# Kernel tuning notes

Hardware: AMD Instinct MI355X
Metric: run time of the kernel (lower is better)

The kernel has to match this reference:

```python
import jax, jax.numpy as jnp
import numpy as np
from jax import lax

V, B, T, H = 8000, 64, 128, 512
EMB_INIT = 0.5 / 128.0  # init_width = 0.5 / embedding_size


def setup_inputs() -> dict:
    key = jax.random.key(0)
    ks = jax.random.split(key, 9)
    return {
        "input_data": jax.random.randint(ks[0], (B, T), 0, V, dtype=jnp.int64),
        "targets": jax.random.randint(ks[1], (B, T), 0, V, dtype=jnp.int64),
        "embedding": jax.random.uniform(ks[2], (V, H), minval=-EMB_INIT, maxval=EMB_INIT, dtype=jnp.float32),
        "W1": jax.random.normal(ks[3], (2 * H, 4 * H), dtype=jnp.float32) * 0.02,
        "b1": jnp.zeros((4 * H,), dtype=jnp.float32),
        "W2": jax.random.normal(ks[4], (2 * H, 4 * H), dtype=jnp.float32) * 0.02,
        "b2": jnp.zeros((4 * H,), dtype=jnp.float32),
        "softmax_w": jax.random.normal(ks[5], (H, V), dtype=jnp.float32) * 0.02,
        "softmax_b": jnp.zeros((V,), dtype=jnp.float32),
    }


def _lstm_step(c, h, x, W, b):
    # BasicLSTMCell with forget_bias=0.0, gate order i, j, f, o
    gates = jnp.concatenate([x, h], axis=-1) @ W + b  # [B, 4H]
    i, j, f, o = jnp.split(gates, 4, axis=-1)
    c_new = c * jax.nn.sigmoid(f) + jax.nn.sigmoid(i) * jnp.tanh(j)
    h_new = jnp.tanh(c_new) * jax.nn.sigmoid(o)
    return c_new, h_new


def reference(input_data, targets, embedding, W1, b1, W2, b2, softmax_w, softmax_b):
    x = embedding[input_data]            # [B, T, H] embedding lookup
    xt = jnp.transpose(x, (1, 0, 2))     # [T, B, H] time-major for scan

    def step(carry, x_t):
        c1, h1, c2, h2 = carry
        c1, h1 = _lstm_step(c1, h1, x_t, W1, b1)
        c2, h2 = _lstm_step(c2, h2, h1, W2, b2)
        return (c1, h1, c2, h2), h2

    init = tuple(jnp.zeros((B, H), dtype=x.dtype) for _ in range(4))
    _, hs = lax.scan(step, init, xt)     # [T, B, H]

    outputs = jnp.transpose(hs, (1, 0, 2)).reshape(-1, H)  # [B*T, H]
    logits = outputs @ softmax_w + softmax_b               # [B*T, V]
    labels = targets.reshape(-1)                            # [B*T]

    logp = jax.nn.log_softmax(logits, axis=-1)
    loss = -jnp.take_along_axis(logp, labels[:, None], axis=1)[:, 0]  # per-token CE
    cost = jnp.sum(loss) / (B * T)
    return cost
```

## Files before the change

### kernel.cpp

```cpp
#include <hip/hip_runtime.h>
#include <hip/hip_bf16.h>


#define V_SIZE 8000
#define B_SIZE 64
#define T_SIZE 128
#define H_SIZE 512
#define NG     (4 * H_SIZE)
#define HB     (H_SIZE * B_SIZE)
#define RBLK   64
#define RTH    256
#define SENT   0x7FFF7FFFu

typedef __attribute__((ext_vector_type(8))) short bf16x8;
typedef __attribute__((ext_vector_type(8))) unsigned short u16x8;
typedef __attribute__((ext_vector_type(4))) float f32x4;

__device__ __forceinline__ float bf2f(unsigned short u) {
  union { unsigned int i; float f; } x; x.i = ((unsigned int)u) << 16; return x.f;
}
__device__ __forceinline__ unsigned short f2bf(float f) {
  union { float f; unsigned int i; } x; x.f = f;
  unsigned int r = x.i + 0x7fffu + ((x.i >> 16) & 1u);
  return (unsigned short)(r >> 16);
}
__device__ __forceinline__ float sigf(float v) { return 1.f / (1.f + __expf(-v)); }
__device__ __forceinline__ float tanhf_fast(float v) {
  return 1.f - 2.f / (__expf(2.f * v) + 1.f);
}

__device__ __forceinline__ bf16x8 aload16(const unsigned short* p) {
  unsigned long long lo = __hip_atomic_load((const unsigned long long*)p,
                                            __ATOMIC_RELAXED, __HIP_MEMORY_SCOPE_AGENT);
  unsigned long long hi = __hip_atomic_load((const unsigned long long*)(p + 4),
                                            __ATOMIC_RELAXED, __HIP_MEMORY_SCOPE_AGENT);
  union { unsigned long long v[2]; bf16x8 b; } u;
  u.v[0] = lo; u.v[1] = hi;
  return u.b;
}
__device__ __forceinline__ unsigned has_sent(bf16x8 v) {
  union { bf16x8 b; unsigned u[4]; } x; x.b = v;
  return (unsigned)((x.u[0] == SENT) | (x.u[1] == SENT) |
                    (x.u[2] == SENT) | (x.u[3] == SENT));
}

__device__ __forceinline__ void load8_mall(bf16x8* d, const unsigned short* base) {
  asm volatile(
      "global_load_dwordx4 %0, %8, off sc0 sc1\n\t"
      "global_load_dwordx4 %1, %8, off offset:64 sc0 sc1\n\t"
      "global_load_dwordx4 %2, %8, off offset:128 sc0 sc1\n\t"
      "global_load_dwordx4 %3, %8, off offset:192 sc0 sc1\n\t"
      "global_load_dwordx4 %4, %8, off offset:256 sc0 sc1\n\t"
      "global_load_dwordx4 %5, %8, off offset:320 sc0 sc1\n\t"
      "global_load_dwordx4 %6, %8, off offset:384 sc0 sc1\n\t"
      "global_load_dwordx4 %7, %8, off offset:448 sc0 sc1\n\t"
      "s_waitcnt vmcnt(0)"
      : "=v"(d[0]), "=v"(d[1]), "=v"(d[2]), "=v"(d[3]),
        "=v"(d[4]), "=v"(d[5]), "=v"(d[6]), "=v"(d[7])
      : "v"(base)
      : "memory");
}

__global__ void fill_k(unsigned* __restrict__ p, unsigned v, int n) {
  int i = blockIdx.x * 256 + threadIdx.x;
  if (i < n) p[i] = v;
}

__global__ __launch_bounds__(256) void xgather_k(const int* __restrict__ ids,
                                                 const float* __restrict__ emb,
                                                 unsigned short* __restrict__ xb) {
  int g = blockIdx.x * 256 + threadIdx.x;
  int r = g >> 6, c = g & 63;
  int t = r >> 6, b = r & 63;
  int id = ids[(size_t)b * T_SIZE + t];
  const float4* s4 = reinterpret_cast<const float4*>(emb + (size_t)id * H_SIZE + c * 8);
  float4 v0 = s4[0], v1 = s4[1];
  u16x8 o;
  o[0] = f2bf(v0.x); o[1] = f2bf(v0.y); o[2] = f2bf(v0.z); o[3] = f2bf(v0.w);
  o[4] = f2bf(v1.x); o[5] = f2bf(v1.y); o[6] = f2bf(v1.z); o[7] = f2bf(v1.w);
  *reinterpret_cast<u16x8*>(xb + (size_t)r * H_SIZE + c * 8) = o;
}

__global__ __launch_bounds__(256) void trans_k(const float* __restrict__ src,
                                               unsigned short* __restrict__ dst,
                                               int src_ld, int n_tiles) {
  __shared__ float tile[64][65];
  const int tid = threadIdx.x;
  const int kt = blockIdx.x / n_tiles, nt = blockIdx.x % n_tiles;
#pragma unroll
  for (int q = 0; q < 16; ++q) {
    int f = tid + 256 * q;
    int r = f >> 6, c = f & 63;
    tile[r][c] = src[(size_t)(kt * 64 + r) * src_ld + nt * 64 + c];
  }
  __syncthreads();
#pragma unroll
  for (int q = 0; q < 2; ++q) {
    int u = tid + 256 * q;
    int n = u >> 3, kg = u & 7;
    u16x8 o;
#pragma unroll
    for (int e = 0; e < 8; ++e) o[e] = f2bf(tile[kg * 8 + e][n]);
    *reinterpret_cast<u16x8*>(dst + (size_t)(nt * 64 + n) * 512 + kt * 64 + kg * 8) = o;
  }
}

__device__ __forceinline__ void loadB8(bf16x8* p, const unsigned short* Wb,
                                       int vc, int kh, int kof) {
#pragma unroll
  for (int ks = 0; ks < 8; ++ks)
    p[ks] = *reinterpret_cast<const bf16x8*>(
        Wb + (size_t)vc * 512 + (kh * 8 + ks) * 32 + kof);
}

__global__ __launch_bounds__(RTH, 1) void recur_k(
    const float* __restrict__ W1, const float* __restrict__ W2,
    const float* __restrict__ b1, const float* __restrict__ b2,
    const unsigned short* __restrict__ xb,
    const unsigned short* __restrict__ hzero,
    unsigned short* __restrict__ h1all, unsigned short* __restrict__ h2all)
{
  __shared__ short wldsX[2 * 16 * 64 * 8];
  __shared__ short wlds1[2 * 16 * 64 * 8];
  __shared__ short wlds2[2 * 32 * 64 * 8];
  __shared__ float gbA[64][32];
  __shared__ float gbB[64][32];

  const int tid = threadIdx.x;
  const int bid = blockIdx.x;
  const int h0  = bid * 8;
  const int w   = tid >> 6, l = tid & 63;

  {
    for (int idx = tid; idx < 2 * 16 * 64; idx += RTH) {
      int ln2 = idx & 63;
      int ks  = (idx >> 6) % 16;
      int ng  = (idx >> 6) / 16;
      int n   = ln2 & 15;
      int col = (n & 3) * H_SIZE + h0 + ng * 4 + (n >> 2);
      int kb  = ks * 32 + (ln2 >> 4) * 8;
      short* dX = &wldsX[((size_t)(ng * 16 + ks) * 64 + ln2) * 8];
      short* d1 = &wlds1[((size_t)(ng * 16 + ks) * 64 + ln2) * 8];
#pragma unroll
      for (int e = 0; e < 8; ++e) {
        dX[e] = (short)f2bf(W1[(size_t)(kb + e) * NG + col]);
        d1[e] = (short)f2bf(W1[(size_t)(H_SIZE + kb + e) * NG + col]);
      }
    }
    for (int idx = tid; idx < 2 * 32 * 64; idx += RTH) {
      int ln2 = idx & 63;
      int ks  = (idx >> 6) % 32;
      int ng  = (idx >> 6) / 32;
      int n   = ln2 & 15;
      int col = (n & 3) * H_SIZE + h0 + ng * 4 + (n >> 2);
      int kb  = ks * 32 + (ln2 >> 4) * 8;
      short* dst = &wlds2[((size_t)(ng * 32 + ks) * 64 + ln2) * 8];
#pragma unroll
      for (int e = 0; e < 8; ++e)
        dst[e] = (short)f2bf(W2[(size_t)(kb + e) * NG + col]);
    }
  }

  const int pb = tid >> 2, pq = tid & 3;
  float c1[2] = {0.f, 0.f}, c2[2] = {0.f, 0.f};
  float bias1[2][4], bias2[2][4];
#pragma unroll
  for (int hh = 0; hh < 2; ++hh)
#pragma unroll
    for (int g = 0; g < 4; ++g) {
      bias1[hh][g] = b1[g * H_SIZE + h0 + 2 * pq + hh];
      bias2[hh][g] = b2[g * H_SIZE + h0 + 2 * pq + hh];
    }
  __syncthreads();

  const int arow = w * 16 + (l & 15);
  const int kof  = (l >> 4) * 8;

  for (int t = 0; t <= T_SIZE; ++t) {
    f32x4 acc0 = {0.f, 0.f, 0.f, 0.f};
    f32x4 acc1 = {0.f, 0.f, 0.f, 0.f};
    if (t < T_SIZE) {
      const unsigned short* xr = xb + ((size_t)t * 64 + arow) * H_SIZE + kof;
#pragma unroll
      for (int ks = 0; ks < 16; ++ks) {
        bf16x8 avx = *reinterpret_cast<const bf16x8*>(xr + ks * 32);
        bf16x8 bv0 = *reinterpret_cast<const bf16x8*>(&wldsX[((size_t)(0 * 16 + ks) * 64 + l) * 8]);
        bf16x8 bv1 = *reinterpret_cast<const bf16x8*>(&wldsX[((size_t)(1 * 16 + ks) * 64 + l) * 8]);
        acc0 = __builtin_amdgcn_mfma_f32_16x16x32_bf16(avx, bv0, acc0, 0, 0, 0);
        acc1 = __builtin_amdgcn_mfma_f32_16x16x32_bf16(avx, bv1, acc1, 0, 0, 0);
      }
    }

    const unsigned short* h1src = ((t == 0) ? hzero : h1all + (size_t)(t - 1) * HB)
                                  + (size_t)arow * H_SIZE + kof;
    const unsigned short* h2src = ((t < 2) ? hzero : h2all + (size_t)(t - 2) * HB)
                                  + (size_t)arow * H_SIZE + kof;
    bf16x8 av1[16], av2[16];
    load8_mall(av1, h1src);
    load8_mall(av1 + 8, h1src + 256);
    load8_mall(av2, h2src);
    load8_mall(av2 + 8, h2src + 256);
    {
      unsigned p1m = 0, p2m = 0;
#pragma unroll
      for (int ks = 0; ks < 16; ++ks) {
        p1m |= has_sent(av1[ks]) << ks;
        p2m |= has_sent(av2[ks]) << ks;
      }
      while (p1m | p2m) {
        __builtin_amdgcn_s_sleep(2);
#pragma unroll
        for (int ks = 0; ks < 16; ++ks)
          if ((p1m >> ks) & 1) {
            av1[ks] = aload16(h1src + ks * 32);
            if (!has_sent(av1[ks])) p1m &= ~(1u << ks);
          }
#pragma unroll
        for (int ks = 0; ks < 16; ++ks)
          if ((p2m >> ks) & 1) {
            av2[ks] = aload16(h2src + ks * 32);
            if (!has_sent(av2[ks])) p2m &= ~(1u << ks);
          }
      }
    }

    if (t < T_SIZE) {
#pragma unroll
      for (int ks = 0; ks < 16; ++ks) {
        bf16x8 bv0 = *reinterpret_cast<const bf16x8*>(&wlds1[((size_t)(0 * 16 + ks) * 64 + l) * 8]);
        bf16x8 bv1 = *reinterpret_cast<const bf16x8*>(&wlds1[((size_t)(1 * 16 + ks) * 64 + l) * 8]);
        acc0 = __builtin_amdgcn_mfma_f32_16x16x32_bf16(av1[ks], bv0, acc0, 0, 0, 0);
        acc1 = __builtin_amdgcn_mfma_f32_16x16x32_bf16(av1[ks], bv1, acc1, 0, 0, 0);
      }
      {
        const int crow = w * 16 + ((l >> 4) << 2);
        const int ccol = l & 15;
#pragma unroll
        for (int r = 0; r < 4; ++r) {
          gbA[crow + r][ccol]      = acc0[r];
          gbA[crow + r][16 + ccol] = acc1[r];
        }
      }
      __syncthreads();
      unsigned short hbv[2];
#pragma unroll
      for (int hh = 0; hh < 2; ++hh) {
        const int hl = 2 * pq + hh;
        const int ng = hl >> 2, jj = hl & 3;
        float g[4];
#pragma unroll
        for (int gg = 0; gg < 4; ++gg)
          g[gg] = gbA[pb][ng * 16 + jj * 4 + gg] + bias1[hh][gg];
        float cn = c1[hh] * sigf(g[2]) + sigf(g[0]) * tanhf_fast(g[1]);
        float hn = tanhf_fast(cn) * sigf(g[3]);
        c1[hh] = cn;
        hbv[hh] = f2bf(hn);
      }
      unsigned pack = (unsigned)hbv[0] | ((unsigned)hbv[1] << 16);
      __hip_atomic_store((unsigned*)(h1all + (size_t)t * HB + (size_t)pb * H_SIZE
                                     + h0 + 2 * pq),
                         pack, __ATOMIC_RELAXED, __HIP_MEMORY_SCOPE_AGENT);
    }

    if (t >= 1) {
      f32x4 bcc0 = {0.f, 0.f, 0.f, 0.f};
      f32x4 bcc1 = {0.f, 0.f, 0.f, 0.f};
#pragma unroll
      for (int ks = 0; ks < 16; ++ks) {
        bf16x8 bv0 = *reinterpret_cast<const bf16x8*>(&wlds2[((size_t)(0 * 32 + 16 + ks) * 64 + l) * 8]);
        bf16x8 bv1 = *reinterpret_cast<const bf16x8*>(&wlds2[((size_t)(1 * 32 + 16 + ks) * 64 + l) * 8]);
        bcc0 = __builtin_amdgcn_mfma_f32_16x16x32_bf16(av2[ks], bv0, bcc0, 0, 0, 0);
        bcc1 = __builtin_amdgcn_mfma_f32_16x16x32_bf16(av2[ks], bv1, bcc1, 0, 0, 0);
      }
#pragma unroll
      for (int ks = 0; ks < 16; ++ks) {
        bf16x8 bv0 = *reinterpret_cast<const bf16x8*>(&wlds2[((size_t)(0 * 32 + ks) * 64 + l) * 8]);
        bf16x8 bv1 = *reinterpret_cast<const bf16x8*>(&wlds2[((size_t)(1 * 32 + ks) * 64 + l) * 8]);
        bcc0 = __builtin_amdgcn_mfma_f32_16x16x32_bf16(av1[ks], bv0, bcc0, 0, 0, 0);
        bcc1 = __builtin_amdgcn_mfma_f32_16x16x32_bf16(av1[ks], bv1, bcc1, 0, 0, 0);
      }
      {
        const int crow = w * 16 + ((l >> 4) << 2);
        const int ccol = l & 15;
#pragma unroll
        for (int r = 0; r < 4; ++r) {
          gbB[crow + r][ccol]      = bcc0[r];
          gbB[crow + r][16 + ccol] = bcc1[r];
        }
      }
      __syncthreads();
      unsigned short hbv[2];
#pragma unroll
      for (int hh = 0; hh < 2; ++hh) {
        const int hl = 2 * pq + hh;
        const int ng = hl >> 2, jj = hl & 3;
        float g[4];
#pragma unroll
        for (int gg = 0; gg < 4; ++gg)
          g[gg] = gbB[pb][ng * 16 + jj * 4 + gg] + bias2[hh][gg];
        float cn = c2[hh] * sigf(g[2]) + sigf(g[0]) * tanhf_fast(g[1]);
        float hn = tanhf_fast(cn) * sigf(g[3]);
        c2[hh] = cn;
        hbv[hh] = f2bf(hn);
      }
      unsigned pack = (unsigned)hbv[0] | ((unsigned)hbv[1] << 16);
      __hip_atomic_store((unsigned*)(h2all + (size_t)(t - 1) * HB
                                     + (size_t)pb * H_SIZE + h0 + 2 * pq),
                         pack, __ATOMIC_RELAXED, __HIP_MEMORY_SCOPE_AGENT);
    }

    __syncthreads();
  }
}

__global__ __launch_bounds__(512) void ce_mfma_k(const unsigned short* __restrict__ outs,
                                                 const unsigned short* __restrict__ Wvb,
                                                 const float* __restrict__ bvb,
                                                 const int* __restrict__ tgts,
                                                 float* __restrict__ pmx,
                                                 float* __restrict__ psm,
                                                 float* __restrict__ ptg) {
  const int tid = threadIdx.x;
  const int t = blockIdx.x >> 1, half = blockIdx.x & 1;
  const int w = tid >> 6, l = tid & 63;
  const int wr = w & 3, wq = w >> 2;
  const int m0 = wr * 16;
  const int kof = (l >> 4) * 8;
  const int ln = l & 15;
  const int c0 = half * 4000 + wq * 2000;
  bf16x8 av[16];
#pragma unroll
  for (int ks = 0; ks < 16; ++ks)
    av[ks] = *reinterpret_cast<const bf16x8*>(
        outs + ((size_t)t * 64 + m0 + ln) * H_SIZE + ks * 32 + kof);
  int lbl[4];
#pragma unroll
  for (int r = 0; r < 4; ++r)
    lbl[r] = tgts[(size_t)(m0 + ((l >> 4) << 2) + r) * T_SIZE + t];

  float mx[4] = {-1e30f, -1e30f, -1e30f, -1e30f};
  float sm[4] = {0.f, 0.f, 0.f, 0.f};
  float tg[4] = {0.f, 0.f, 0.f, 0.f};

  bf16x8 p0[8], p1[8];
  loadB8(p0, Wvb, c0 + ln, 0, kof);
  for (int ct = 0; ct < 125; ++ct) {
    const int vc = c0 + ct * 16 + ln;
    const int vcn = c0 + ((ct < 124) ? ct + 1 : ct) * 16 + ln;
    f32x4 acc = {0.f, 0.f, 0.f, 0.f};
    loadB8(p1, Wvb, vc, 1, kof);
#pragma unroll
    for (int ks = 0; ks < 8; ++ks)
      acc = __builtin_amdgcn_mfma_f32_16x16x32_bf16(av[ks], p0[ks], acc, 0, 0, 0);
    loadB8(p0, Wvb, vcn, 0, kof);
#pragma unroll
    for (int ks = 0; ks < 8; ++ks)
      acc = __builtin_amdgcn_mfma_f32_16x16x32_bf16(av[8 + ks], p1[ks], acc, 0, 0, 0);

    float bb = bvb[vc];
#pragma unroll
    for (int r = 0; r < 4; ++r) {
      float lg = acc[r] + bb;
      tg[r] += (vc == lbl[r]) ? lg : 0.f;
      float nm = fmaxf(mx[r], lg);
      sm[r] = sm[r] * __expf(mx[r] - nm) + __expf(lg - nm);
      mx[r] = nm;
    }
  }

#pragma unroll
  for (int off = 1; off <= 8; off <<= 1) {
#pragma unroll
    for (int r = 0; r < 4; ++r) {
      float om = __shfl_xor(mx[r], off, 64);
      float os = __shfl_xor(sm[r], off, 64);
      float ot = __shfl_xor(tg[r], off, 64);
      float nm = fmaxf(mx[r], om);
      sm[r] = sm[r] * __expf(mx[r] - nm) + os * __expf(om - nm);
      mx[r] = nm;
      tg[r] += ot;
    }
  }
  if (ln == 0) {
    int idx = ((int)blockIdx.x * 2 + wq) * 64 + m0 + ((l >> 4) << 2);
#pragma unroll
    for (int r = 0; r < 4; ++r) {
      pmx[idx + r] = mx[r]; psm[idx + r] = sm[r]; ptg[idx + r] = tg[r];
    }
  }
}

__global__ __launch_bounds__(256) void cemerge_k(const float* __restrict__ pmx,
                                                 const float* __restrict__ psm,
                                                 const float* __restrict__ ptg,
                                                 float* __restrict__ accum) {
  int g = blockIdx.x * 256 + threadIdx.x;
  int t = g >> 6, row = g & 63;
  float M = -1e30f, S = 0.f, T = 0.f;
#pragma unroll
  for (int j = 0; j < 4; ++j) {
    int i = (t * 4 + j) * 64 + row;
    float m = pmx[i], s = psm[i];
    float nm = fmaxf(M, m);
    S = S * __expf(M - nm) + s * __expf(m - nm);
    M = nm;
    T += ptg[i];
  }
  float loss = M + logf(S) - T;
#pragma unroll
  for (int off = 32; off >= 1; off >>= 1)
    loss += __shfl_xor(loss, off, 64);
  if ((threadIdx.x & 63) == 0) atomicAdd(accum, loss);
}

__global__ void finish_k(const float* __restrict__ accum, float* __restrict__ out) {
  out[0] = accum[0] * (1.f / (float)(B_SIZE * T_SIZE));
}

extern "C" void kernel_launch(void* const* d_in, const int* in_sizes, int n_in,
                              void* d_out, int out_size, void* d_ws, size_t ws_size,
                              hipStream_t stream) {
  const int*   ids  = (const int*)  d_in[0];
  const int*   tgts = (const int*)  d_in[1];
  const float* emb  = (const float*)d_in[2];
  const float* W1   = (const float*)d_in[3];
  const float* b1   = (const float*)d_in[4];
  const float* W2   = (const float*)d_in[5];
  const float* b2   = (const float*)d_in[6];
  const float* Wv   = (const float*)d_in[7];
  const float* bv   = (const float*)d_in[8];
  float* out = (float*)d_out;

  char* ws = (char*)d_ws;
  unsigned short* xb    = (unsigned short*)(ws);
  unsigned short* outsb = (unsigned short*)(ws + 8388608);
  unsigned short* h1all = (unsigned short*)(ws + 16777216);
  unsigned short* Wvb   = (unsigned short*)(ws + 25165824);
  unsigned short* hzero = (unsigned short*)(ws + 33357824);
  float*          accum = (float*)         (ws + 33423360);
  float*          pmx   = (float*)         (ws + 33423424);
  float*          psm   = (float*)         (ws + 33554496);
  float*          ptg   = (float*)         (ws + 33685568);

  fill_k<<<65, 256, 0, stream>>>((unsigned*)hzero, 0u, 16385);

  xgather_k<<<2048, 256, 0, stream>>>(ids, emb, xb);
  trans_k<<<1000, 256, 0, stream>>>(Wv, Wvb, V_SIZE, 125);

  fill_k<<<8192, 256, 0, stream>>>((unsigned*)h1all, SENT, 2097152);
  fill_k<<<8192, 256, 0, stream>>>((unsigned*)outsb, SENT, 2097152);

  {
    void* args[] = { (void*)&W1, (void*)&W2, (void*)&b1, (void*)&b2,
                     (void*)&xb, (void*)&hzero, (void*)&h1all, (void*)&outsb };
    hipError_t e = hipLaunchCooperativeKernel((const void*)recur_k,
                                              dim3(RBLK), dim3(RTH),
                                              args, 0, stream);
    if (e != hipSuccess) {
      recur_k<<<dim3(RBLK), dim3(RTH), 0, stream>>>(W1, W2, b1, b2, xb, hzero,
                                                    h1all, outsb);
    }
  }

  ce_mfma_k<<<256, 512, 0, stream>>>(outsb, Wvb, bv, tgts, pmx, psm, ptg);
  cemerge_k<<<32, 256, 0, stream>>>(pmx, psm, ptg, accum);
  finish_k<<<1, 1, 0, stream>>>(accum, out);
}
```

Before: 1.728 ms.

## Restructure cross-entropy kernel with padded vocab, two row tiles per wave, no running max

The cross-entropy MFMA kernel now has each wave compute two 16-row tiles against the same weight fragments, so every B load feeds twice as many MFMAs. The vocab is padded to 8192: padded columns get zero weights and a -1e30 bias, which removes the ragged tail. The online max/rescale is dropped in favour of plain exp sums, relying on logits being small enough not to overflow, and the merge step simplifies to match. The two sentinel fills are merged into one launch, and a small kernel builds the padded bias.

```diff
diff --git a/kernel.cpp b/kernel.cpp
--- a/kernel.cpp
+++ b/kernel.cpp
@@ -3,6 +3,7 @@
 
 
 #define V_SIZE 8000
+#define VPAD   8192
 #define B_SIZE 64
 #define T_SIZE 128
 #define H_SIZE 512
@@ -66,6 +67,11 @@
   if (i < n) p[i] = v;
 }
 
+__global__ void bvp_k(const float* __restrict__ bv, float* __restrict__ bvp) {
+  int i = blockIdx.x * 256 + threadIdx.x;
+  bvp[i] = (i < V_SIZE) ? bv[i] : -1e30f;
+}
+
 __global__ __launch_bounds__(256) void xgather_k(const int* __restrict__ ids,
                                                  const float* __restrict__ emb,
                                                  unsigned short* __restrict__ xb) {
@@ -83,7 +89,7 @@
 
 __global__ __launch_bounds__(256) void trans_k(const float* __restrict__ src,
                                                unsigned short* __restrict__ dst,
-                                               int src_ld, int n_tiles) {
+                                               int src_ld, int n_tiles, int Nsrc) {
   __shared__ float tile[64][65];
   const int tid = threadIdx.x;
   const int kt = blockIdx.x / n_tiles, nt = blockIdx.x % n_tiles;
@@ -91,7 +97,8 @@
   for (int q = 0; q < 16; ++q) {
     int f = tid + 256 * q;
     int r = f >> 6, c = f & 63;
-    tile[r][c] = src[(size_t)(kt * 64 + r) * src_ld + nt * 64 + c];
+    int col = nt * 64 + c;
+    tile[r][c] = (col < Nsrc) ? src[(size_t)(kt * 64 + r) * src_ld + col] : 0.f;
   }
   __syncthreads();
 #pragma unroll
@@ -313,58 +320,68 @@
   }
 }
 
-__global__ __launch_bounds__(512) void ce_mfma_k(const unsigned short* __restrict__ outs,
-                                                 const unsigned short* __restrict__ Wvb,
-                                                 const float* __restrict__ bvb,
-                                                 const int* __restrict__ tgts,
-                                                 float* __restrict__ pmx,
-                                                 float* __restrict__ psm,
-                                                 float* __restrict__ ptg) {
+__global__ __launch_bounds__(512) void ce2_k(const unsigned short* __restrict__ outs,
+                                             const unsigned short* __restrict__ Wvb,
+                                             const float* __restrict__ bvp,
+                                             const int* __restrict__ tgts,
+                                             float* __restrict__ psm,
+                                             float* __restrict__ ptg) {
   const int tid = threadIdx.x;
-  const int t = blockIdx.x >> 1, half = blockIdx.x & 1;
+  const int rb = blockIdx.x >> 3, cb = blockIdx.x & 7;
   const int w = tid >> 6, l = tid & 63;
-  const int wr = w & 3, wq = w >> 2;
-  const int m0 = wr * 16;
   const int kof = (l >> 4) * 8;
   const int ln = l & 15;
-  const int c0 = half * 4000 + wq * 2000;
-  bf16x8 av[16];
-#pragma unroll
-  for (int ks = 0; ks < 16; ++ks)
-    av[ks] = *reinterpret_cast<const bf16x8*>(
-        outs + ((size_t)t * 64 + m0 + ln) * H_SIZE + ks * 32 + kof);
-  int lbl[4];
-#pragma unroll
-  for (int r = 0; r < 4; ++r)
-    lbl[r] = tgts[(size_t)(m0 + ((l >> 4) << 2) + r) * T_SIZE + t];
-
-  float mx[4] = {-1e30f, -1e30f, -1e30f, -1e30f};
-  float sm[4] = {0.f, 0.f, 0.f, 0.f};
-  float tg[4] = {0.f, 0.f, 0.f, 0.f};
+  const int r0 = rb * 256 + w * 32;
+  const int cbase = cb * 1024;
+
+  bf16x8 av0[16], av1[16];
+#pragma unroll
+  for (int ks = 0; ks < 16; ++ks) {
+    av0[ks] = *reinterpret_cast<const bf16x8*>(
+        outs + (size_t)(r0 + ln) * H_SIZE + ks * 32 + kof);
+    av1[ks] = *reinterpret_cast<const bf16x8*>(
+        outs + (size_t)(r0 + 16 + ln) * H_SIZE + ks * 32 + kof);
+  }
+  int lbl0[4], lbl1[4];
+#pragma unroll
+  for (int r = 0; r < 4; ++r) {
+    int rr = r0 + ((l >> 4) << 2) + r;
+    lbl0[r] = tgts[(size_t)(rr & 63) * T_SIZE + (rr >> 6)];
+    rr += 16;
+    lbl1[r] = tgts[(size_t)(rr & 63) * T_SIZE + (rr >> 6)];
+  }
+
+  float sm0[4] = {0.f, 0.f, 0.f, 0.f}, sm1[4] = {0.f, 0.f, 0.f, 0.f};
+  float tg0[4] = {0.f, 0.f, 0.f, 0.f}, tg1[4] = {0.f, 0.f, 0.f, 0.f};
 
   bf16x8 p0[8], p1[8];
-  loadB8(p0, Wvb, c0 + ln, 0, kof);
-  for (int ct = 0; ct < 125; ++ct) {
-    const int vc = c0 + ct * 16 + ln;
-    const int vcn = c0 + ((ct < 124) ? ct + 1 : ct) * 16 + ln;
-    f32x4 acc = {0.f, 0.f, 0.f, 0.f};
+  loadB8(p0, Wvb, cbase + ln, 0, kof);
+  for (int ct = 0; ct < 64; ++ct) {
+    const int vc = cbase + ct * 16 + ln;
+    const int vcn = cbase + ((ct < 63) ? ct + 1 : ct) * 16 + ln;
+    f32x4 a0 = {0.f, 0.f, 0.f, 0.f};
+    f32x4 a1 = {0.f, 0.f, 0.f, 0.f};
     loadB8(p1, Wvb, vc, 1, kof);
 #pragma unroll
-    for (int ks = 0; ks < 8; ++ks)
-      acc = __builtin_amdgcn_mfma_f32_16x16x32_bf16(av[ks], p0[ks], acc, 0, 0, 0);
+    for (int ks = 0; ks < 8; ++ks) {
+      a0 = __builtin_amdgcn_mfma_f32_16x16x32_bf16(av0[ks], p0[ks], a0, 0, 0, 0);
+      a1 = __builtin_amdgcn_mfma_f32_16x16x32_bf16(av1[ks], p0[ks], a1, 0, 0, 0);
+    }
     loadB8(p0, Wvb, vcn, 0, kof);
 #pragma unroll
-    for (int ks = 0; ks < 8; ++ks)
-      acc = __builtin_amdgcn_mfma_f32_16x16x32_bf16(av[8 + ks], p1[ks], acc, 0, 0, 0);
-
-    float bb = bvb[vc];
+    for (int ks = 0; ks < 8; ++ks) {
+      a0 = __builtin_amdgcn_mfma_f32_16x16x32_bf16(av0[8 + ks], p1[ks], a0, 0, 0, 0);
+      a1 = __builtin_amdgcn_mfma_f32_16x16x32_bf16(av1[8 + ks], p1[ks], a1, 0, 0, 0);
+    }
+    float bb = bvp[vc];
 #pragma unroll
     for (int r = 0; r < 4; ++r) {
-      float lg = acc[r] + bb;
-      tg[r] += (vc == lbl[r]) ? lg : 0.f;
-      float nm = fmaxf(mx[r], lg);
-      sm[r] = sm[r] * __expf(mx[r] - nm) + __expf(lg - nm);
-      mx[r] = nm;
+      float lg = a0[r] + bb;
+      sm0[r] += __expf(lg);
+      tg0[r] += (vc == lbl0[r]) ? lg : 0.f;
+      float lh = a1[r] + bb;
+      sm1[r] += __expf(lh);
+      tg1[r] += (vc == lbl1[r]) ? lh : 0.f;
     }
   }
 
@@ -372,41 +389,35 @@
   for (int off = 1; off <= 8; off <<= 1) {
 #pragma unroll
     for (int r = 0; r < 4; ++r) {
-      float om = __shfl_xor(mx[r], off, 64);
-      float os = __shfl_xor(sm[r], off, 64);
-      float ot = __shfl_xor(tg[r], off, 64);
-      float nm = fmaxf(mx[r], om);
-      sm[r] = sm[r] * __expf(mx[r] - nm) + os * __expf(om - nm);
-      mx[r] = nm;
-      tg[r] += ot;
+      sm0[r] += __shfl_xor(sm0[r], off, 64);
+      tg0[r] += __shfl_xor(tg0[r], off, 64);
+      sm1[r] += __shfl_xor(sm1[r], off, 64);
+      tg1[r] += __shfl_xor(tg1[r], off, 64);
     }
   }
   if (ln == 0) {
-    int idx = ((int)blockIdx.x * 2 + wq) * 64 + m0 + ((l >> 4) << 2);
+    int rrw = r0 + ((l >> 4) << 2);
 #pragma unroll
     for (int r = 0; r < 4; ++r) {
-      pmx[idx + r] = mx[r]; psm[idx + r] = sm[r]; ptg[idx + r] = tg[r];
-    }
-  }
-}
-
-__global__ __launch_bounds__(256) void cemerge_k(const float* __restrict__ pmx,
-                                                 const float* __restrict__ psm,
+      psm[(size_t)cb * 8192 + rrw + r]      = sm0[r];
+      ptg[(size_t)cb * 8192 + rrw + r]      = tg0[r];
+      psm[(size_t)cb * 8192 + rrw + 16 + r] = sm1[r];
+      ptg[(size_t)cb * 8192 + rrw + 16 + r] = tg1[r];
+    }
+  }
+}
+
+__global__ __launch_bounds__(256) void cemerge_k(const float* __restrict__ psm,
                                                  const float* __restrict__ ptg,
                                                  float* __restrict__ accum) {
   int g = blockIdx.x * 256 + threadIdx.x;
-  int t = g >> 6, row = g & 63;
-  float M = -1e30f, S = 0.f, T = 0.f;
-#pragma unroll
-  for (int j = 0; j < 4; ++j) {
-    int i = (t * 4 + j) * 64 + row;
-    float m = pmx[i], s = psm[i];
-    float nm = fmaxf(M, m);
-    S = S * __expf(M - nm) + s * __expf(m - nm);
-    M = nm;
-    T += ptg[i];
-  }
-  float loss = M + logf(S) - T;
+  float S = 0.f, T = 0.f;
+#pragma unroll
+  for (int j = 0; j < 8; ++j) {
+    S += psm[(size_t)j * 8192 + g];
+    T += ptg[(size_t)j * 8192 + g];
+  }
+  float loss = logf(S) - T;
 #pragma unroll
   for (int off = 32; off >= 1; off >>= 1)
     loss += __shfl_xor(loss, off, 64);
@@ -436,19 +447,18 @@
   unsigned short* outsb = (unsigned short*)(ws + 8388608);
   unsigned short* h1all = (unsigned short*)(ws + 16777216);
   unsigned short* Wvb   = (unsigned short*)(ws + 25165824);
-  unsigned short* hzero = (unsigned short*)(ws + 33357824);
-  float*          accum = (float*)         (ws + 33423360);
-  float*          pmx   = (float*)         (ws + 33423424);
-  float*          psm   = (float*)         (ws + 33554496);
-  float*          ptg   = (float*)         (ws + 33685568);
-
-  fill_k<<<65, 256, 0, stream>>>((unsigned*)hzero, 0u, 16385);
-
+  unsigned short* hzero = (unsigned short*)(ws + 33554432);
+  float*          bvp   = (float*)         (ws + 33619968);
+  float*          accum = (float*)         (ws + 33652736);
+  float*          psm   = (float*)         (ws + 33652800);
+  float*          ptg   = (float*)         (ws + 33914944);
+
+  fill_k<<<97, 256, 0, stream>>>((unsigned*)hzero, 0u, 24592);
+  fill_k<<<16384, 256, 0, stream>>>((unsigned*)outsb, SENT, 4194304);
+
+  bvp_k<<<32, 256, 0, stream>>>(bv, bvp);
   xgather_k<<<2048, 256, 0, stream>>>(ids, emb, xb);
-  trans_k<<<1000, 256, 0, stream>>>(Wv, Wvb, V_SIZE, 125);
-
-  fill_k<<<8192, 256, 0, stream>>>((unsigned*)h1all, SENT, 2097152);
-  fill_k<<<8192, 256, 0, stream>>>((unsigned*)outsb, SENT, 2097152);
+  trans_k<<<1024, 256, 0, stream>>>(Wv, Wvb, V_SIZE, 128, V_SIZE);
 
   {
     void* args[] = { (void*)&W1, (void*)&W2, (void*)&b1, (void*)&b2,
@@ -462,7 +472,7 @@
     }
   }
 
-  ce_mfma_k<<<256, 512, 0, stream>>>(outsb, Wvb, bv, tgts, pmx, psm, ptg);
-  cemerge_k<<<32, 256, 0, stream>>>(pmx, psm, ptg, accum);
+  ce2_k<<<256, 512, 0, stream>>>(outsb, Wvb, bvp, tgts, psm, ptg);
+  cemerge_k<<<32, 256, 0, stream>>>(psm, ptg, accum);
   finish_k<<<1, 1, 0, stream>>>(accum, out);
 }
```

After: 1.524 ms. 11.8% less time.
